# Kernel tuning notes

Measured on AMD Instinct MI355X. Metric: run time of the kernel, lower is better.

The kernel has to match this reference:

```python
import jax, jax.numpy as jnp
import numpy as np

DIM = 2048
NHEADS = 32
HEAD_DIM = DIM // NHEADS
EPS = 1e-6


def _rmsnorm(t):
    # RMSNorm over last dim, no weight
    return t * jax.lax.rsqrt(jnp.mean(t * t, axis=-1, keepdims=True) + EPS)


def setup_inputs() -> dict:
    key = jax.random.key(0)
    kx, kc, kq, kk, kv = jax.random.split(key, 5)
    x = jax.random.normal(kx, (2, 4096, DIM), dtype=jnp.float32)
    context = jax.random.normal(kc, (2, 512, DIM), dtype=jnp.float32)
    std = 0.02
    Wq = jax.random.normal(kq, (DIM, DIM), dtype=jnp.float32) * std
    Wk = jax.random.normal(kk, (DIM, DIM), dtype=jnp.float32) * std
    Wv = jax.random.normal(kv, (DIM, DIM), dtype=jnp.float32) * std
    return {"x": x, "context": context, "Wq": Wq, "Wk": Wk, "Wv": Wv}


def reference(x, context, Wq, Wk, Wv):
    b, n, _ = x.shape
    m = context.shape[1]
    # projections (torch Linear: y = x @ W.T, no bias)
    q = x @ Wq.T                      # (b, n, dim)
    k_raw = context @ Wk.T            # (b, m, dim)
    v_raw = context @ Wv.T            # (b, m, dim)

    # split q into heads: b n (h d) -> b h n d
    q = q.reshape(b, n, NHEADS, HEAD_DIM).transpose(0, 2, 1, 3)

    # faithful to the original: cat(k,v) then 'b n (h d j)' with j=2
    kv = jnp.concatenate([k_raw, v_raw], axis=-1)          # (b, m, 2*dim)
    kv = kv.reshape(b, m, NHEADS, HEAD_DIM, 2)             # (h d j) factorization
    k = kv[..., 0].transpose(0, 2, 1, 3)                   # (b, h, m, d)
    v = kv[..., 1].transpose(0, 2, 1, 3)                   # (b, h, m, d)

    # per-head QK RMSNorm (no weight)
    q = _rmsnorm(q)
    k = _rmsnorm(k)

    scale = HEAD_DIM ** -0.5
    scores = jnp.einsum('bhnd,bhmd->bhnm', q, k) * scale
    attn = jax.nn.softmax(scores, axis=-1)
    out = jnp.einsum('bhnm,bhmd->bhnd', attn, v)           # (b, h, n, d)
    # back to (b, n, dim)
    return out.transpose(0, 2, 1, 3).reshape(b, n, NHEADS * HEAD_DIM)
```

## Files before the change

### kernel.cpp

```cpp
#include <hip/hip_runtime.h>
#include <cstdint>


typedef unsigned short u16;
typedef unsigned int u32;
typedef __bf16 bf16x8 __attribute__((ext_vector_type(8)));
typedef float f32x4 __attribute__((ext_vector_type(4)));
typedef float f32x16 __attribute__((ext_vector_type(16)));

__device__ __forceinline__ u16 f2bf(float f) {
  union { float f; unsigned u; } a; a.f = f;
  unsigned r = a.u + 0x7FFFu + ((a.u >> 16) & 1u);
  return (u16)(r >> 16);
}

__device__ __forceinline__ void gload_lds16(const u16* g, u16* l) {
  __builtin_amdgcn_global_load_lds((const __attribute__((address_space(1))) void*)g,
                                   (__attribute__((address_space(3))) void*)l, 16, 0, 0);
}

__global__ __launch_bounds__(256) void cvt_bf16(const float4* __restrict__ in,
                                                uint2* __restrict__ out, int n4) {
  int i = blockIdx.x * 256 + threadIdx.x;
  if (i >= n4) return;
  float4 v = in[i];
  uint2 o;
  o.x = (unsigned)f2bf(v.x) | ((unsigned)f2bf(v.y) << 16);
  o.y = (unsigned)f2bf(v.z) | ((unsigned)f2bf(v.w) << 16);
  out[i] = o;
}

__global__ __launch_bounds__(512, 2) void qgemm256(const u16* __restrict__ A,
                                                   const u16* __restrict__ B,
                                                   u16* __restrict__ QN) {
  constexpr int K = 2048, T = 32;
  __shared__ __align__(16) u16 As[2][256 * 64];
  __shared__ __align__(16) u16 Bs[2][256 * 64];
  const int t = threadIdx.x;
  const int wid = t >> 6, l = t & 63;
  const int wr = wid >> 2, wc = wid & 3;
  const int lr = l & 15, lg = l >> 4;
  const int bid = blockIdx.x;
  const int bx = bid >> 3, by = bid & 7;
  const int brow = bx << 8, bcol = by << 8;

  const int srcu = ((l & 7) ^ (l >> 3)) << 3;
  const int growA = brow + (wid << 3) + (l >> 3);
  const int growB = bcol + (wid << 3) + (l >> 3);

  const int u2k0 = ((lg ^ (l & 7)) << 3);
  const int u2k1 = u2k0 ^ 32;
  const int rbA = (((wr << 7) + lr) << 6);
  const int rbB = (((wc << 6) + lr) << 6);

  f32x4 acc[8][4] = {};

  auto stage = [&](int buf, int half, int kto, bool isB) {
    const u16* gp = isB ? B : A;
    const int grow = (isB ? growB : growA) + (half << 7);
    u16* lb = (isB ? Bs[buf] : As[buf]) + (half << 13) + (wid << 9);
#pragma unroll
    for (int i = 0; i < 2; ++i)
      gload_lds16(gp + (size_t)(grow + (i << 6)) * K + kto + srcu, lb + (i << 12));
  };

  stage(0, 0, 0, false); stage(0, 1, 0, false);
  stage(0, 0, 0, true);  stage(0, 1, 0, true);
  asm volatile("s_waitcnt vmcnt(0)" ::: "memory");
  __builtin_amdgcn_s_barrier();

  for (int tt = 0; tt < T; ++tt) {
    const int bufc = tt & 1, bufn = bufc ^ 1;
    const int kto = (tt + 1) << 6;
    const bool pre = (tt + 1 < T);

    if (pre) {
      stage(bufn, 0, kto, false);
      asm volatile("s_waitcnt vmcnt(2)" ::: "memory");
    } else {
      asm volatile("s_waitcnt vmcnt(0)" ::: "memory");
    }
    __builtin_amdgcn_sched_barrier(0);
    __builtin_amdgcn_s_barrier();

    bf16x8 bfr[4][2];
#pragma unroll
    for (int ni = 0; ni < 4; ++ni) {
      bfr[ni][0] = *(const bf16x8*)&Bs[bufc][rbB + (ni << 10) + u2k0];
      bfr[ni][1] = *(const bf16x8*)&Bs[bufc][rbB + (ni << 10) + u2k1];
    }
    {
      bf16x8 af[2][2];
#pragma unroll
      for (int j = 0; j < 2; ++j) {
        af[j][0] = *(const bf16x8*)&As[bufc][rbA + (j << 10) + u2k0];
        af[j][1] = *(const bf16x8*)&As[bufc][rbA + (j << 10) + u2k1];
      }
      asm volatile("s_waitcnt lgkmcnt(0)" ::: "memory");
      __builtin_amdgcn_sched_barrier(0);
      __builtin_amdgcn_s_setprio(1);
#pragma unroll
      for (int j = 0; j < 2; ++j)
#pragma unroll
        for (int ni = 0; ni < 4; ++ni)
#pragma unroll
          for (int kk = 0; kk < 2; ++kk)
            acc[j][ni] = __builtin_amdgcn_mfma_f32_16x16x32_bf16(
                af[j][kk], bfr[ni][kk], acc[j][ni], 0, 0, 0);
      __builtin_amdgcn_s_setprio(0);
      __builtin_amdgcn_sched_barrier(0);
      __builtin_amdgcn_s_barrier();
    }

#pragma unroll
    for (int p = 1; p < 4; ++p) {
      const int mi0 = p << 1;
      bf16x8 af[2][2];
#pragma unroll
      for (int j = 0; j < 2; ++j) {
        af[j][0] = *(const bf16x8*)&As[bufc][rbA + ((mi0 + j) << 10) + u2k0];
        af[j][1] = *(const bf16x8*)&As[bufc][rbA + ((mi0 + j) << 10) + u2k1];
      }
      if (pre) {
        if (p == 1) stage(bufn, 1, kto, false);
        else stage(bufn, p - 2, kto, true);
      }
      __builtin_amdgcn_sched_barrier(0);
      __builtin_amdgcn_s_barrier();
      asm volatile("s_waitcnt lgkmcnt(0)" ::: "memory");
      __builtin_amdgcn_sched_barrier(0);
      __builtin_amdgcn_s_setprio(1);
#pragma unroll
      for (int j = 0; j < 2; ++j)
#pragma unroll
        for (int ni = 0; ni < 4; ++ni)
#pragma unroll
          for (int kk = 0; kk < 2; ++kk)
            acc[mi0 + j][ni] = __builtin_amdgcn_mfma_f32_16x16x32_bf16(
                af[j][kk], bfr[ni][kk], acc[mi0 + j][ni], 0, 0, 0);
      __builtin_amdgcn_s_setprio(0);
      __builtin_amdgcn_sched_barrier(0);
      __builtin_amdgcn_s_barrier();
    }
  }

  const int head = (by << 2) + wc;
#pragma unroll
  for (int mi = 0; mi < 8; ++mi) {
#pragma unroll
    for (int r = 0; r < 4; ++r) {
      float ss = 0.f;
#pragma unroll
      for (int ni = 0; ni < 4; ++ni) { float v = acc[mi][ni][r]; ss += v * v; }
      ss += __shfl_xor(ss, 1); ss += __shfl_xor(ss, 2);
      ss += __shfl_xor(ss, 4); ss += __shfl_xor(ss, 8);
      const float sc = rsqrtf(ss * (1.f / 64.f) + 1e-6f) * (0.125f * 1.4426950408889634f);
      const int row = brow + (wr << 7) + (mi << 4) + (lg << 2) + r;
      const int b = row >> 12, n = row & 4095;
      u16* o = QN + ((size_t)((b << 5) + head) * 4096 + n) * 64;
#pragma unroll
      for (int ni = 0; ni < 4; ++ni)
        o[(ni << 4) + lr] = f2bf(acc[mi][ni][r] * sc);
    }
  }
}

__global__ __launch_bounds__(256) void gemm_bt(const u16* __restrict__ A,
                                               const u16* __restrict__ B,
                                               float* __restrict__ C, int ldc) {
  constexpr int K = 2048;
  __shared__ __align__(16) u16 As[128 * 32];
  __shared__ __align__(16) u16 Bs[128 * 32];
  const int t = threadIdx.x;
  const int w = t >> 6, l = t & 63;
  const int wr = w >> 1, wc = w & 1;
  const int lr = l & 15, lg = l >> 4;
  const int brow = blockIdx.x << 7, bcol = blockIdx.y << 7;

  f32x4 acc[4][4] = {};

  const int c0 = (w << 6) + l;
  const u16* Ab = A + (size_t)brow * K;
  const u16* Bb = B + (size_t)bcol * K;

  for (int kt = 0; kt < K; kt += 32) {
    __syncthreads();
#pragma unroll
    for (int i = 0; i < 2; ++i) {
      const int c = (i << 8) + c0;
      const int row = c >> 2, koff = (c & 3) << 3;
      gload_lds16(Ab + (size_t)row * K + kt + koff, As + (((i << 8) + (w << 6)) << 3));
      gload_lds16(Bb + (size_t)row * K + kt + koff, Bs + (((i << 8) + (w << 6)) << 3));
    }
    __syncthreads();
    bf16x8 af[4], bfr[4];
#pragma unroll
    for (int mi = 0; mi < 4; ++mi)
      af[mi] = *(const bf16x8*)&As[(((wr << 6) + (mi << 4) + lr) << 5) + (lg << 3)];
#pragma unroll
    for (int ni = 0; ni < 4; ++ni)
      bfr[ni] = *(const bf16x8*)&Bs[(((wc << 6) + (ni << 4) + lr) << 5) + (lg << 3)];
#pragma unroll
    for (int mi = 0; mi < 4; ++mi)
#pragma unroll
      for (int ni = 0; ni < 4; ++ni)
        acc[mi][ni] = __builtin_amdgcn_mfma_f32_16x16x32_bf16(af[mi], bfr[ni], acc[mi][ni], 0, 0, 0);
  }

#pragma unroll
  for (int mi = 0; mi < 4; ++mi)
#pragma unroll
    for (int r = 0; r < 4; ++r) {
      const int row = brow + (wr << 6) + (mi << 4) + (lg << 2) + r;
      float* o = C + (size_t)row * ldc + bcol + (wc << 6);
#pragma unroll
      for (int ni = 0; ni < 4; ++ni)
        o[(ni << 4) + lr] = acc[mi][ni][r];
    }
}

__global__ __launch_bounds__(256) void kvbuild2(const float* __restrict__ kv,
                                                u16* __restrict__ kn,
                                                u16* __restrict__ vtn) {
  __shared__ u16 Vl[64][72];
  const int t = threadIdx.x;
  const int bh = blockIdx.x >> 3, mt = blockIdx.x & 7;
  const int b = bh >> 5, h = bh & 31;
  const int mloc = t >> 2, dc = (t & 3) << 4;
  const int m = (mt << 6) + mloc;
  const float2* src = (const float2*)(kv + ((size_t)((b << 9) + m)) * 4096 + ((h >> 4) << 11))
                      + ((h & 15) << 6) + dc;
  float kvals[16], vvals[16];
  float ss = 0.f;
#pragma unroll
  for (int dd = 0; dd < 16; ++dd) {
    float2 p = src[dd];
    kvals[dd] = p.x; vvals[dd] = p.y;
    ss += p.x * p.x;
  }
  ss += __shfl_xor(ss, 1); ss += __shfl_xor(ss, 2);
  const float sc = rsqrtf(ss * (1.f / 64.f) + 1e-6f);
  union { uint4 u4[2]; u16 h[16]; } ko;
#pragma unroll
  for (int dd = 0; dd < 16; ++dd) ko.h[dd] = f2bf(kvals[dd] * sc);
  u16* kdst = kn + ((size_t)bh * 512 + m) * 64 + dc;
  *(uint4*)kdst = ko.u4[0];
  *(uint4*)(kdst + 8) = ko.u4[1];
#pragma unroll
  for (int dd = 0; dd < 16; ++dd) Vl[dc + dd][mloc] = f2bf(vvals[dd]);
  __syncthreads();
  const int drow = t >> 2, mc = (t & 3) << 4;
  uint4 r0 = *(const uint4*)&Vl[drow][mc];
  uint4 r1 = *(const uint4*)&Vl[drow][mc + 8];
  u16* vdst = vtn + ((size_t)(bh << 6) + drow) * 512 + (mt << 6) + mc;
  *(uint4*)vdst = r0;
  *(uint4*)(vdst + 8) = r1;
}

__global__ __launch_bounds__(256) void attn2(const u16* __restrict__ qn,
                                             const u16* __restrict__ kn,
                                             const u16* __restrict__ vtn,
                                             float* __restrict__ out) {
  __shared__ __align__(16) u16 Kt[64 * 72];
  __shared__ __align__(16) u16 Vt[64 * 72];
  const int t = threadIdx.x, w = t >> 6, l = t & 63;
  const int i31 = l & 31, hi = l >> 5;
  const int nblk = blockIdx.x, bh = blockIdx.y;
  const int b = bh >> 5, h = bh & 31;
  const int qrow = (nblk << 7) + (w << 5) + i31;

  const u16* qb = qn + ((size_t)bh * 4096 + qrow) * 64 + (hi << 3);
  bf16x8 bq[4];
#pragma unroll
  for (int kt = 0; kt < 4; ++kt) bq[kt] = *(const bf16x8*)(qb + (kt << 4));

  f32x16 po[2];
#pragma unroll
  for (int d = 0; d < 2; ++d)
#pragma unroll
    for (int r = 0; r < 16; ++r) po[d][r] = 0.f;
  float mrun = -3e38f, lrun = 0.f;

  const u16* kb = kn + ((size_t)bh << 9) * 64;
  const u16* vb = vtn + ((size_t)bh << 6) * 512;
  const int srow = t >> 2, sp = (t & 3) << 3;

  for (int mt = 0; mt < 8; ++mt) {
    __syncthreads();
    {
      const u16* gk = kb + (size_t)((mt << 6) + srow) * 64 + sp;
      uint4 a0 = *(const uint4*)gk;
      uint4 a1 = *(const uint4*)(gk + 32);
      const u16* gv = vb + (size_t)srow * 512 + (mt << 6) + sp;
      uint4 b0 = *(const uint4*)gv;
      uint4 b1 = *(const uint4*)(gv + 32);
      *(uint4*)&Kt[srow * 72 + sp] = a0;
      *(uint4*)&Kt[srow * 72 + sp + 32] = a1;
      *(uint4*)&Vt[srow * 72 + sp] = b0;
      *(uint4*)&Vt[srow * 72 + sp + 32] = b1;
    }
    __syncthreads();

    f32x16 fs[2];
#pragma unroll
    for (int jt = 0; jt < 2; ++jt) {
      f32x16 s = {};
#pragma unroll
      for (int kt = 0; kt < 4; ++kt) {
        const bf16x8 ak = *(const bf16x8*)&Kt[((jt << 5) + i31) * 72 + (kt << 4) + (hi << 3)];
        s = __builtin_amdgcn_mfma_f32_32x32x16_bf16(ak, bq[kt], s, 0, 0, 0);
      }
      fs[jt] = s;
    }

    float pm = fs[0][0];
#pragma unroll
    for (int r = 1; r < 16; ++r) pm = fmaxf(pm, fs[0][r]);
#pragma unroll
    for (int r = 0; r < 16; ++r) pm = fmaxf(pm, fs[1][r]);
    pm = fmaxf(pm, __shfl_xor(pm, 32));
    if (!__all(pm <= mrun + 8.f)) {
      const float mnew = fmaxf(mrun, pm);
      const float corr = exp2f(mrun - mnew);
      lrun *= corr;
#pragma unroll
      for (int d = 0; d < 2; ++d)
#pragma unroll
        for (int r = 0; r < 16; ++r) po[d][r] *= corr;
      mrun = mnew;
    }
    float rs = 0.f;
    u32 pq[2][4][2];
#pragma unroll
    for (int jt = 0; jt < 2; ++jt)
#pragma unroll
      for (int q = 0; q < 4; ++q)
#pragma unroll
        for (int rp = 0; rp < 2; ++rp) {
          const float p0 = exp2f(fs[jt][(q << 2) + (rp << 1)] - mrun);
          const float p1 = exp2f(fs[jt][(q << 2) + (rp << 1) + 1] - mrun);
          rs += p0 + p1;
          union { u32 u; __bf16 h2[2]; } pk;
          pk.h2[0] = (__bf16)p0;
          pk.h2[1] = (__bf16)p1;
          pq[jt][q][rp] = pk.u;
        }
    rs += __shfl_xor(rs, 32);
    lrun += rs;

#pragma unroll
    for (int kk = 0; kk < 4; ++kk) {
      const int jt = kk >> 1, q0 = (kk & 1) << 1;
      union { u32 wd[4]; bf16x8 v; } pf;
#pragma unroll
      for (int rp = 0; rp < 2; ++rp) {
        const u32 v0 = pq[jt][q0][rp], v1 = pq[jt][q0 + 1][rp];
        const u32 send = hi ? v0 : v1;
        const u32 ex = (u32)__shfl_xor((int)send, 32);
        pf.wd[rp] = hi ? ex : v0;
        pf.wd[2 + rp] = hi ? v1 : ex;
      }
#pragma unroll
      for (int dt = 0; dt < 2; ++dt) {
        const bf16x8 av = *(const bf16x8*)&Vt[((dt << 5) + i31) * 72 + (kk << 4) + (hi << 3)];
        po[dt] = __builtin_amdgcn_mfma_f32_32x32x16_bf16(av, pf.v, po[dt], 0, 0, 0);
      }
    }
  }

  const float inv = 1.f / lrun;
  float* ob = out + ((size_t)(b << 12) + qrow) * 2048 + (h << 6) + (hi << 2);
#pragma unroll
  for (int dt = 0; dt < 2; ++dt)
#pragma unroll
    for (int q = 0; q < 4; ++q) {
      float4 v = { po[dt][(q << 2)] * inv, po[dt][(q << 2) + 1] * inv,
                   po[dt][(q << 2) + 2] * inv, po[dt][(q << 2) + 3] * inv };
      *(float4*)(ob + (dt << 5) + (q << 3)) = v;
    }
}

extern "C" void kernel_launch(void* const* d_in, const int* in_sizes, int n_in,
                              void* d_out, int out_size, void* d_ws, size_t ws_size,
                              hipStream_t stream) {
  const float* x   = (const float*)d_in[0];
  const float* ctx = (const float*)d_in[1];
  const float* Wq  = (const float*)d_in[2];
  const float* Wk  = (const float*)d_in[3];
  const float* Wv  = (const float*)d_in[4];
  float* out = (float*)d_out;
  char* ws = (char*)d_ws;

  u16* xb   = (u16*)(ws + 0);
  u16* cb   = (u16*)(ws + 33554432);
  u16* Wqb  = (u16*)(ws + 37748736);
  u16* Wkb  = (u16*)(ws + 46137344);
  u16* Wvb  = (u16*)(ws + 54525952);
  u16* qnp  = (u16*)(ws + 62914560);
  float* kvraw = (float*)(ws + 0);
  u16* knp  = (u16*)(ws + 16777216);
  u16* vtnp = (u16*)(ws + 20971520);

  cvt_bf16<<<16384, 256, 0, stream>>>((const float4*)x,   (uint2*)xb,  4194304);
  cvt_bf16<<<2048,  256, 0, stream>>>((const float4*)ctx, (uint2*)cb,   524288);
  cvt_bf16<<<4096,  256, 0, stream>>>((const float4*)Wq,  (uint2*)Wqb, 1048576);
  cvt_bf16<<<4096,  256, 0, stream>>>((const float4*)Wk,  (uint2*)Wkb, 1048576);
  cvt_bf16<<<4096,  256, 0, stream>>>((const float4*)Wv,  (uint2*)Wvb, 1048576);

  qgemm256<<<256, 512, 0, stream>>>(xb, Wqb, qnp);
  gemm_bt<<<dim3(8, 32), 256, 0, stream>>>(cb, Wkb, kvraw, 4096);
  kvbuild2<<<512, 256, 0, stream>>>(kvraw, knp, vtnp);
  attn2<<<dim3(32, 64), 256, 0, stream>>>(qnp, knp, vtnp, out);
}
```

Measured before the change: 381.1 us.

## Issue all next-tile loads upfront and drop per-phase barriers in GEMM loop

The Q-projection GEMM main loop now issues all four global-to-LDS stage loads for the next K tile at the start of the iteration instead of spreading them across the four MFMA phases. It then runs the four MFMA groups back to back, with no interleaved barriers, setprio toggles or explicit lgkmcnt waits, and keeps a single barrier at the end. This is meant to cut synchronisation overhead and let the compiler schedule LDS reads and MFMAs freely. The cost is a burstier memory issue pattern and less explicit control over instruction interleaving.

```diff
diff --git a/kernel.cpp b/kernel.cpp
--- a/kernel.cpp
+++ b/kernel.cpp
@@ -75,13 +75,15 @@
     const bool pre = (tt + 1 < T);
 
     if (pre) {
-      stage(bufn, 0, kto, false);
-      asm volatile("s_waitcnt vmcnt(2)" ::: "memory");
+      stage(bufn, 0, kto, false); stage(bufn, 1, kto, false);
+      stage(bufn, 0, kto, true);  stage(bufn, 1, kto, true);
+      asm volatile("s_waitcnt vmcnt(8)" ::: "memory");
     } else {
       asm volatile("s_waitcnt vmcnt(0)" ::: "memory");
     }
     __builtin_amdgcn_sched_barrier(0);
     __builtin_amdgcn_s_barrier();
+    __builtin_amdgcn_sched_barrier(0);
 
     bf16x8 bfr[4][2];
 #pragma unroll
@@ -89,59 +91,26 @@
       bfr[ni][0] = *(const bf16x8*)&Bs[bufc][rbB + (ni << 10) + u2k0];
       bfr[ni][1] = *(const bf16x8*)&Bs[bufc][rbB + (ni << 10) + u2k1];
     }
-    {
+#pragma unroll
+    for (int g = 0; g < 4; ++g) {
       bf16x8 af[2][2];
 #pragma unroll
       for (int j = 0; j < 2; ++j) {
-        af[j][0] = *(const bf16x8*)&As[bufc][rbA + (j << 10) + u2k0];
-        af[j][1] = *(const bf16x8*)&As[bufc][rbA + (j << 10) + u2k1];
+        af[j][0] = *(const bf16x8*)&As[bufc][rbA + (((g << 1) + j) << 10) + u2k0];
+        af[j][1] = *(const bf16x8*)&As[bufc][rbA + (((g << 1) + j) << 10) + u2k1];
       }
-      asm volatile("s_waitcnt lgkmcnt(0)" ::: "memory");
-      __builtin_amdgcn_sched_barrier(0);
-      __builtin_amdgcn_s_setprio(1);
 #pragma unroll
       for (int j = 0; j < 2; ++j)
 #pragma unroll
         for (int ni = 0; ni < 4; ++ni)
 #pragma unroll
           for (int kk = 0; kk < 2; ++kk)
-            acc[j][ni] = __builtin_amdgcn_mfma_f32_16x16x32_bf16(
-                af[j][kk], bfr[ni][kk], acc[j][ni], 0, 0, 0);
-      __builtin_amdgcn_s_setprio(0);
-      __builtin_amdgcn_sched_barrier(0);
-      __builtin_amdgcn_s_barrier();
-    }
-
-#pragma unroll
-    for (int p = 1; p < 4; ++p) {
-      const int mi0 = p << 1;
-      bf16x8 af[2][2];
-#pragma unroll
-      for (int j = 0; j < 2; ++j) {
-        af[j][0] = *(const bf16x8*)&As[bufc][rbA + ((mi0 + j) << 10) + u2k0];
-        af[j][1] = *(const bf16x8*)&As[bufc][rbA + ((mi0 + j) << 10) + u2k1];
-      }
-      if (pre) {
-        if (p == 1) stage(bufn, 1, kto, false);
-        else stage(bufn, p - 2, kto, true);
-      }
-      __builtin_amdgcn_sched_barrier(0);
-      __builtin_amdgcn_s_barrier();
-      asm volatile("s_waitcnt lgkmcnt(0)" ::: "memory");
-      __builtin_amdgcn_sched_barrier(0);
-      __builtin_amdgcn_s_setprio(1);
-#pragma unroll
-      for (int j = 0; j < 2; ++j)
-#pragma unroll
-        for (int ni = 0; ni < 4; ++ni)
-#pragma unroll
-          for (int kk = 0; kk < 2; ++kk)
-            acc[mi0 + j][ni] = __builtin_amdgcn_mfma_f32_16x16x32_bf16(
-                af[j][kk], bfr[ni][kk], acc[mi0 + j][ni], 0, 0, 0);
-      __builtin_amdgcn_s_setprio(0);
-      __builtin_amdgcn_sched_barrier(0);
-      __builtin_amdgcn_s_barrier();
-    }
+            acc[(g << 1) + j][ni] = __builtin_amdgcn_mfma_f32_16x16x32_bf16(
+                af[j][kk], bfr[ni][kk], acc[(g << 1) + j][ni], 0, 0, 0);
+    }
+
+    __builtin_amdgcn_sched_barrier(0);
+    __builtin_amdgcn_s_barrier();
   }
 
   const int head = (by << 2) + wc;
```

Result: faster. 369.1 us (-3.2%).
